# Kernel optimization log

Hardware: AMD Instinct MI355X
Metric: run time of the kernel (lower is better)

Reference implementation:

```python
import jax, jax.numpy as jnp
import numpy as np

N_NODES, N_EDGES, B = 5000, 160000, 8
IN_DIM, NB, RH = 64, 8, 64
MUL0, MUL1, MUL2 = 32, 16, 8
NW = 144  # 32*3 + 16*2 + 8*2 tensor-product path weights per edge
R_MAX, AVG_NEI = 6.0, 32.0
NL, POOL_H, OUT_D = 4, 128, 512


def setup_inputs():
    ks = jax.random.split(jax.random.key(0), 24)
    f = lambda k, shape, scale=1.0: jax.random.normal(k, shape, jnp.float32) * scale
    return {
        "x": f(ks[0], (N_NODES, IN_DIM)),
        "pos": f(ks[1], (N_NODES, 3)),
        "W_in": f(ks[2], (IN_DIM, MUL0), IN_DIM ** -0.5),
        "Wr1": f(ks[3], (NL, NB, RH), NB ** -0.5), "br1": jnp.zeros((NL, RH)),
        "Wr2": f(ks[4], (NL, RH, RH), RH ** -0.5), "br2": jnp.zeros((NL, RH)),
        "Wr3": f(ks[5], (NL, RH, NW), RH ** -0.5), "br3": jnp.zeros((NL, NW)),
        "Wm0": f(ks[6], (NL, 56, MUL0), 56 ** -0.5),
        "Wm1": f(ks[7], (NL, 48, MUL1), 48 ** -0.5),
        "Wm2": f(ks[8], (NL, 40, MUL2), 40 ** -0.5),
        "Ws0": f(ks[9], (NL, MUL0, MUL0), MUL0 ** -0.5),
        "Ws1": f(ks[10], (NL, MUL1, MUL1), MUL1 ** -0.5),
        "Ws2": f(ks[11], (NL, MUL2, MUL2), MUL2 ** -0.5),
        "Wg": f(ks[12], (NL, MUL0, MUL1 + MUL2), MUL0 ** -0.5), "bg": jnp.zeros((NL, MUL1 + MUL2)),
        "Wp1": f(ks[13], (MUL0, POOL_H), MUL0 ** -0.5), "bp1": jnp.zeros((POOL_H,)),
        "Wp2": f(ks[14], (POOL_H, POOL_H), POOL_H ** -0.5), "bp2": jnp.zeros((POOL_H,)),
        "Wp3": f(ks[15], (POOL_H, 1), POOL_H ** -0.5), "bp3": jnp.zeros((1,)),
        "Wo1": f(ks[16], (MUL0, OUT_D * 2), MUL0 ** -0.5), "bo1": jnp.zeros((OUT_D * 2,)),
        "g1": jnp.ones((OUT_D * 2,)), "be1": jnp.zeros((OUT_D * 2,)),
        "Wo2": f(ks[17], (OUT_D * 2, OUT_D), (OUT_D * 2) ** -0.5), "bo2": jnp.zeros((OUT_D,)),
        "g2": jnp.ones((OUT_D,)), "be2": jnp.zeros((OUT_D,)),
        "edge_index": jax.random.randint(ks[18], (2, N_EDGES), 0, N_NODES),
        "batch": jnp.sort(jax.random.randint(ks[19], (N_NODES,), 0, B)),
    }


def _ln(x, gamma, beta):
    m = x.mean(-1, keepdims=True)
    v = x.var(-1, keepdims=True)
    return (x - m) / jnp.sqrt(v + 1e-5) * gamma + beta


def _forward(x, pos, W_in, Wr1, br1, Wr2, br2, Wr3, br3, Wm0, Wm1, Wm2,
             Ws0, Ws1, Ws2, Wg, bg, Wp1, bp1, Wp2, bp2, Wp3, bp3,
             Wo1, bo1, g1, be1, Wo2, bo2, g2, be2, edge_index, batch):
    N = x.shape[0]
    src, dst = edge_index[0], edge_index[1]
    vec = pos[src] - pos[dst]                       # [E,3]
    r = jnp.sqrt(jnp.sum(vec * vec, -1) + 1e-12)    # [E]
    u = vec / r[:, None]
    # Bessel radial basis with smooth polynomial cutoff (p=6)
    nfreq = jnp.arange(1, NB + 1, dtype=x.dtype)
    bess = jnp.sqrt(2.0 / R_MAX) * jnp.sin(nfreq * jnp.pi * r[:, None] / R_MAX) / r[:, None]
    t = jnp.clip(r / R_MAX, 0.0, 1.0)
    fcut = (1.0 - 28.0 * t**6 + 48.0 * t**7 - 21.0 * t**8) * (r < R_MAX).astype(x.dtype)
    edge_emb = bess * fcut[:, None]                 # [E,NB]
    # real spherical harmonics of edge direction, component normalization
    ux, uy, uz = u[:, 0], u[:, 1], u[:, 2]
    Y1 = jnp.sqrt(3.0) * u                          # [E,3]
    Y2 = jnp.stack([15.0**0.5 * ux * uy, 15.0**0.5 * uy * uz,
                    0.5 * 5.0**0.5 * (3.0 * uz * uz - 1.0),
                    15.0**0.5 * ux * uz, 0.5 * 15.0**0.5 * (ux * ux - uy * uy)], -1)  # [E,5]
    # input embedding: 64x0e -> hidden irreps (only scalar path exists; l>0 start at 0)
    s = x @ W_in                                    # [N,32]
    v = jnp.zeros((N, MUL1, 3), x.dtype)            # [N,16,3] 1o
    q = jnp.zeros((N, MUL2, 5), x.dtype)            # [N,8,5]  2e
    for i in range(NL):
        w = jax.nn.silu(edge_emb @ Wr1[i] + br1[i])
        w = jax.nn.silu(w @ Wr2[i] + br2[i])
        w = w @ Wr3[i] + br3[i]                     # [E,144] per-edge TP path weights
        w_ss, w_sv, w_sq, w_vs, w_vv, w_qs, w_qq = jnp.split(w, [32, 64, 96, 112, 128, 136], -1)
        se, ve, qe = s[src], v[src], q[src]         # gather
        # tensor-product messages, grouped by output irrep
        m0 = jnp.concatenate([w_ss * se,
                              w_vv * jnp.einsum('ecm,em->ec', ve, Y1) / 3.0**0.5,
                              w_qq * jnp.einsum('ecm,em->ec', qe, Y2) / 5.0**0.5], -1)   # [E,56]
        m1 = jnp.concatenate([(w_sv * se)[:, :, None] * Y1[:, None, :],
                              w_vs[:, :, None] * ve], 1)                                  # [E,48,3]
        m2 = jnp.concatenate([(w_sq * se)[:, :, None] * Y2[:, None, :],
                              w_qs[:, :, None] * qe], 1)                                  # [E,40,5]
        a0 = jax.ops.segment_sum(m0, dst, num_segments=N) / AVG_NEI
        a1 = jax.ops.segment_sum(m1, dst, num_segments=N) / AVG_NEI
        a2 = jax.ops.segment_sum(m2, dst, num_segments=N) / AVG_NEI
        # per-irrep linear mix + self-connection
        ns = a0 @ Wm0[i] + s @ Ws0[i]
        nv = jnp.einsum('ncm,co->nom', a1, Wm1[i]) + jnp.einsum('ncm,co->nom', v, Ws1[i])
        nq = jnp.einsum('ncm,co->nom', a2, Wm2[i]) + jnp.einsum('ncm,co->nom', q, Ws2[i])
        # gate activation + resnet
        gates = jax.nn.sigmoid(ns @ Wg[i] + bg[i])  # [N,24]
        s = s + jax.nn.silu(ns)
        v = v + nv * gates[:, :MUL1, None]
        q = q + nq * gates[:, MUL1:, None]
    # attention pooling over scalar channels (scatter-softmax per graph)
    logits = (jax.nn.silu(jax.nn.silu(s @ Wp1 + bp1) @ Wp2 + bp2) @ Wp3 + bp3)[:, 0]
    mx = jax.ops.segment_max(logits, batch, num_segments=B)
    z = jnp.exp(logits - mx[batch])
    att = z / jax.ops.segment_sum(z, batch, num_segments=B)[batch]
    gpool = jax.ops.segment_sum(s * att[:, None], batch, num_segments=B)  # [B,32]
    h = jax.nn.silu(_ln(gpool @ Wo1 + bo1, g1, be1))
    return _ln(h @ Wo2 + bo2, g2, be2)              # [B,512]


def reference(x, pos, W_in, Wr1, br1, Wr2, br2, Wr3, br3, Wm0, Wm1, Wm2,
              Ws0, Ws1, Ws2, Wg, bg, Wp1, bp1, Wp2, bp2, Wp3, bp3,
              Wo1, bo1, g1, be1, Wo2, bo2, g2, be2, edge_index, batch):
    return _forward(x, pos, W_in, Wr1, br1, Wr2, br2, Wr3, br3, Wm0, Wm1, Wm2,
                    Ws0, Ws1, Ws2, Wg, bg, Wp1, bp1, Wp2, bp2, Wp3, bp3,
                    Wo1, bo1, g1, be1, Wo2, bo2, g2, be2, edge_index, batch)
```

## Files before the change

kernel.cpp:

```cpp
#include <hip/hip_runtime.h>

constexpr int NN  = 5000;
constexpr int NE  = 160000;
constexpr int NB_ = 8;
constexpr float RMAX   = 6.0f;
constexpr float INV_AVG = 1.0f/32.0f;
constexpr float SQ3  = 1.7320508075688772f;
constexpr float ISQ3 = 0.5773502691896258f;
constexpr float ISQ5 = 0.4472135954999579f;
constexpr float SQ15 = 3.872983346207417f;
constexpr float SQ5  = 2.2360679774997896f;
constexpr float PIF  = 3.14159265358979323846f;

__device__ __forceinline__ float sigmoid_f(float x){
    return 1.0f / (1.0f + __expf(-x));
}
__device__ __forceinline__ float silu_f(float x){ return x * sigmoid_f(x); }

__global__ void k_geom(const float* __restrict__ pos, const int* __restrict__ ei,
                       float* __restrict__ geom, int* __restrict__ counts){
    int e = blockIdx.x*256 + threadIdx.x;
    if (e >= NE) return;
    int s = ei[e], d = ei[NE + e];
    float vx = pos[3*s]-pos[3*d], vy = pos[3*s+1]-pos[3*d+1], vz = pos[3*s+2]-pos[3*d+2];
    float r2 = vx*vx + vy*vy + vz*vz + 1e-12f;
    float r  = sqrtf(r2);
    float ir = 1.0f/r;
    float ux = vx*ir, uy = vy*ir, uz = vz*ir;
    float t  = fminf(r*(1.0f/RMAX), 1.0f);
    float t2=t*t, t3=t2*t, t6=t3*t3, t7=t6*t, t8=t7*t;
    float fc = (1.0f - 28.0f*t6 + 48.0f*t7 - 21.0f*t8) * (r < RMAX ? 1.0f : 0.0f);
    float cb = sqrtf(2.0f/RMAX) * ir * fc;
    float w[16];
    #pragma unroll
    for (int k=0;k<8;k++){
        float arg = (float)(k+1) * (PIF/RMAX) * r;
        w[k] = cb * sinf(arg);
    }
    w[8]  = SQ3*ux; w[9] = SQ3*uy; w[10] = SQ3*uz;
    w[11] = SQ15*ux*uy; w[12] = SQ15*uy*uz; w[13] = 0.5f*SQ5*(3.0f*uz*uz-1.0f);
    w[14] = SQ15*ux*uz; w[15] = 0.5f*SQ15*(ux*ux-uy*uy);
    float4* o = (float4*)(geom + (size_t)e*16);
    o[0] = make_float4(w[0],w[1],w[2],w[3]);
    o[1] = make_float4(w[4],w[5],w[6],w[7]);
    o[2] = make_float4(w[8],w[9],w[10],w[11]);
    o[3] = make_float4(w[12],w[13],w[14],w[15]);
    atomicAdd(&counts[d], 1);
}

__global__ void k_scan(int* __restrict__ cr, int* __restrict__ fpos){
    __shared__ int part[256];
    int t = threadIdx.x;
    const int CH = (NN + 255)/256;
    int base = t*CH;
    int s = 0;
    for (int i=0;i<CH;i++){ int idx = base+i; if (idx < NN) s += cr[idx]; }
    part[t] = s; __syncthreads();
    for (int off=1; off<256; off<<=1){
        int v = (t >= off) ? part[t-off] : 0;
        __syncthreads();
        part[t] += v;
        __syncthreads();
    }
    int run = (t==0) ? 0 : part[t-1];
    for (int i=0;i<CH;i++){
        int idx = base+i;
        if (idx < NN){
            int c = cr[idx];
            cr[idx]  = run;
            fpos[idx] = run;
            run += c;
        } else if (idx == NN){
            cr[idx] = run;
        }
    }
}

__global__ void k_fill(const int* __restrict__ ei, int* __restrict__ fpos,
                       int* __restrict__ elist, int* __restrict__ slot){
    int e = blockIdx.x*256 + threadIdx.x;
    if (e >= NE) return;
    int d = ei[NE+e];
    int p = atomicAdd(&fpos[d], 1);
    elist[p] = e;
    slot[e]  = p;
}

__global__ void k_sinit(const float* __restrict__ x, const float* __restrict__ Win,
                        float* __restrict__ sA){
    int tid = blockIdx.x*256 + threadIdx.x;
    int n = tid >> 5, o = tid & 31;
    if (n >= NN) return;
    float a = 0.f;
    #pragma unroll
    for (int k=0;k<64;k++) a = fmaf(x[n*64+k], Win[k*32+o], a);
    sA[n*32+o] = a;
}

__launch_bounds__(256, 4)
__global__ void k_mlp(const float* __restrict__ geom, const int* __restrict__ slot,
                      const float* __restrict__ Wr1, const float* __restrict__ br1,
                      const float* __restrict__ Wr2, const float* __restrict__ br2,
                      const float* __restrict__ Wr3, const float* __restrict__ br3,
                      float* __restrict__ wbuf, int layer){
    __shared__ __align__(16) float w1s[8*64];
    __shared__ __align__(16) float w2s[64*64];
    __shared__ __align__(16) float b1s[64], b2s[64];
    __shared__ __align__(16) float b3s[144];
    __shared__ __align__(16) float embs[64][8];
    __shared__ __align__(16) float hs[64][68];
    __shared__ int   slots[64];

    const int t  = threadIdx.x;
    const int e0 = blockIdx.x * 64;
    const float* W1 = Wr1 + layer*(8*64);
    const float* b1 = br1 + layer*64;
    const float* W2 = Wr2 + layer*(64*64);
    const float* b2 = br2 + layer*64;
    const float* W3 = Wr3 + layer*(64*144);
    const float* b3 = br3 + layer*144;

    {
        const float4* W2v = (const float4*)W2;
        float4* w2v = (float4*)w2s;
        #pragma unroll
        for (int i=0;i<4;i++) w2v[t + 256*i] = W2v[t + 256*i];
        if (t < 128) ((float4*)w1s)[t] = ((const float4*)W1)[t];
        if (t < 64){ b1s[t] = b1[t]; b2s[t] = b2[t]; slots[t] = slot[e0 + t]; }
        if (t < 144) b3s[t] = b3[t];
        if (t < 128){
            ((float4*)embs)[t] = *((const float4*)geom + (size_t)(e0 + (t>>1))*4 + (t&1));
        }
    }
    __syncthreads();

    const int eg = t >> 3;
    const int jg = t & 7;
    const int ea = eg*2, eb = ea+1;

    float a0[2][8];
    #pragma unroll
    for (int i=0;i<2;i++)
        #pragma unroll
        for (int u=0;u<8;u++) a0[i][u] = b1s[8*jg+u];
    #pragma unroll
    for (int k=0;k<8;k++){
        float e_a = embs[ea][k], e_b = embs[eb][k];
        #pragma unroll
        for (int u=0;u<8;u++){
            float wv = w1s[k*64 + 8*jg + u];
            a0[0][u] = fmaf(e_a, wv, a0[0][u]);
            a0[1][u] = fmaf(e_b, wv, a0[1][u]);
        }
    }
    #pragma unroll
    for (int i=0;i<2;i++){
        int e = ea + i;
        float4 p0 = make_float4(silu_f(a0[i][0]), silu_f(a0[i][1]), silu_f(a0[i][2]), silu_f(a0[i][3]));
        float4 p1 = make_float4(silu_f(a0[i][4]), silu_f(a0[i][5]), silu_f(a0[i][6]), silu_f(a0[i][7]));
        *(float4*)&hs[e][8*jg]     = p0;
        *(float4*)&hs[e][8*jg + 4] = p1;
    }
    __syncthreads();

    float a1[2][8];
    #pragma unroll
    for (int i=0;i<2;i++)
        #pragma unroll
        for (int u=0;u<8;u++) a1[i][u] = b2s[8*jg+u];
    #pragma unroll
    for (int k=0;k<64;k++){
        float h_a = hs[ea][k], h_b = hs[eb][k];
        float4 wA = *(const float4*)&w2s[k*64 + 8*jg];
        float4 wB = *(const float4*)&w2s[k*64 + 8*jg + 4];
        a1[0][0]=fmaf(h_a,wA.x,a1[0][0]); a1[0][1]=fmaf(h_a,wA.y,a1[0][1]);
        a1[0][2]=fmaf(h_a,wA.z,a1[0][2]); a1[0][3]=fmaf(h_a,wA.w,a1[0][3]);
        a1[0][4]=fmaf(h_a,wB.x,a1[0][4]); a1[0][5]=fmaf(h_a,wB.y,a1[0][5]);
        a1[0][6]=fmaf(h_a,wB.z,a1[0][6]); a1[0][7]=fmaf(h_a,wB.w,a1[0][7]);
        a1[1][0]=fmaf(h_b,wA.x,a1[1][0]); a1[1][1]=fmaf(h_b,wA.y,a1[1][1]);
        a1[1][2]=fmaf(h_b,wA.z,a1[1][2]); a1[1][3]=fmaf(h_b,wA.w,a1[1][3]);
        a1[1][4]=fmaf(h_b,wB.x,a1[1][4]); a1[1][5]=fmaf(h_b,wB.y,a1[1][5]);
        a1[1][6]=fmaf(h_b,wB.z,a1[1][6]); a1[1][7]=fmaf(h_b,wB.w,a1[1][7]);
    }
    __syncthreads();
    #pragma unroll
    for (int i=0;i<2;i++){
        int e = ea + i;
        float4 p0 = make_float4(silu_f(a1[i][0]), silu_f(a1[i][1]), silu_f(a1[i][2]), silu_f(a1[i][3]));
        float4 p1 = make_float4(silu_f(a1[i][4]), silu_f(a1[i][5]), silu_f(a1[i][6]), silu_f(a1[i][7]));
        *(float4*)&hs[e][8*jg]     = p0;
        *(float4*)&hs[e][8*jg + 4] = p1;
    }
    __syncthreads();

    float c2[2][18];
    #pragma unroll
    for (int i=0;i<2;i++)
        #pragma unroll
        for (int u=0;u<18;u++) c2[i][u] = b3s[18*jg+u];

    float* w3c = w2s;
    for (int ch=0; ch<4; ++ch){
        const float4* src = (const float4*)(W3 + 16*ch*144);
        float4* dst = (float4*)w3c;
        dst[t]       = src[t];
        dst[t+256]   = src[t+256];
        if (t < 64) dst[t+512] = src[t+512];
        __syncthreads();
        #pragma unroll
        for (int kk=0;kk<16;kk++){
            int k = 16*ch + kk;
            float h_a = hs[ea][k], h_b = hs[eb][k];
            #pragma unroll
            for (int u2=0;u2<9;u2++){
                float2 wv = *(const float2*)&w3c[kk*144 + 18*jg + 2*u2];
                c2[0][2*u2]   = fmaf(h_a, wv.x, c2[0][2*u2]);
                c2[0][2*u2+1] = fmaf(h_a, wv.y, c2[0][2*u2+1]);
                c2[1][2*u2]   = fmaf(h_b, wv.x, c2[1][2*u2]);
                c2[1][2*u2+1] = fmaf(h_b, wv.y, c2[1][2*u2+1]);
            }
        }
        __syncthreads();
    }
    #pragma unroll
    for (int i=0;i<2;i++){
        float* wo = wbuf + (size_t)slots[ea+i]*144 + 18*jg;
        #pragma unroll
        for (int u2=0;u2<9;u2++)
            *(float2*)(wo + 2*u2) = make_float2(c2[i][2*u2], c2[i][2*u2+1]);
    }
}

__launch_bounds__(512, 4)
__global__ void k_gather(const int* __restrict__ rowp, const int* __restrict__ elist,
                         const int* __restrict__ ei, const float* __restrict__ geom,
                         const float* __restrict__ wbuf,
                         const float* __restrict__ s_in, const float* __restrict__ v_in,
                         const float* __restrict__ q_in,
                         float* __restrict__ s_out, float* __restrict__ v_out,
                         float* __restrict__ q_out,
                         const float* __restrict__ Wm0, const float* __restrict__ Wm1,
                         const float* __restrict__ Wm2,
                         const float* __restrict__ Ws0, const float* __restrict__ Ws1,
                         const float* __restrict__ Ws2,
                         const float* __restrict__ Wg, const float* __restrict__ bg,
                         int layer){
    __shared__ float pacc[8][400];
    __shared__ float lacc[400];
    __shared__ float lns[32];
    __shared__ float lgate[24];
    const int n = blockIdx.x;
    const int t = threadIdx.x;
    const int w = t >> 6;
    const int lane = t & 63;

    int s0_w, s0_o, s0_ob;
    if (lane < 32){ s0_w = lane;            s0_o = lane;          s0_ob = lane; }
    else if (lane < 48){ s0_w = 112+(lane-32); s0_o = 3*(lane-32); s0_ob = lane; }
    else if (lane < 56){ s0_w = 136+(lane-48); s0_o = 5*(lane-48); s0_ob = lane; }
    else { int R = lane-56; s0_w = 32+R; s0_o = R; s0_ob = 56+3*R; }
    int s1_w, s1_o, s1_ob;
    if (lane < 24){ int R = lane+8; s1_w = 32+R; s1_o = R;     s1_ob = 56+3*R; }
    else if (lane < 40){ int j = lane-24; s1_w = 96+j; s1_o = 3*j; s1_ob = 152+3*j; }
    else { int R = lane-40; s1_w = 64+R; s1_o = R; s1_ob = 200+5*R; }
    int s2_w, s2_o, s2_ob;
    if (lane < 8){ int R = lane+24; s2_w = 64+R; s2_o = R;   s2_ob = 200+5*R; }
    else { int j = lane-8; s2_w = 128+j; s2_o = 5*j; s2_ob = 360+5*j; }

    float a0[3] = {0.f,0.f,0.f};
    float a1[5] = {0.f,0.f,0.f,0.f,0.f};
    float a2[5] = {0.f,0.f,0.f,0.f,0.f};

    auto body = [&](int idx){
        int e   = elist[idx];
        int src = ei[e];
        const float* gp = geom + (size_t)e*16;
        float4 y14 = *(const float4*)(gp + 8);
        float4 y58 = *(const float4*)(gp + 12);
        const float* wp = wbuf + (size_t)idx*144;
        const float* sp = s_in + (size_t)src*32;
        const float* vp = v_in + (size_t)src*48;
        const float* qp = q_in + (size_t)src*40;
        {
            float wv = wp[s0_w];
            if (lane < 32){
                a0[0] = fmaf(wv, sp[s0_o], a0[0]);
            } else if (lane < 48){
                float dv = vp[s0_o]*y14.x + vp[s0_o+1]*y14.y + vp[s0_o+2]*y14.z;
                a0[0] = fmaf(wv*ISQ3, dv, a0[0]);
            } else if (lane < 56){
                float dq = qp[s0_o]*y14.w + qp[s0_o+1]*y58.x + qp[s0_o+2]*y58.y
                         + qp[s0_o+3]*y58.z + qp[s0_o+4]*y58.w;
                a0[0] = fmaf(wv*ISQ5, dq, a0[0]);
            } else {
                float tmp = wv * sp[s0_o];
                a0[0] = fmaf(tmp, y14.x, a0[0]);
                a0[1] = fmaf(tmp, y14.y, a0[1]);
                a0[2] = fmaf(tmp, y14.z, a0[2]);
            }
        }
        {
            float wv = wp[s1_w];
            if (lane < 24){
                float tmp = wv * sp[s1_o];
                a1[0] = fmaf(tmp, y14.x, a1[0]);
                a1[1] = fmaf(tmp, y14.y, a1[1]);
                a1[2] = fmaf(tmp, y14.z, a1[2]);
            } else if (lane < 40){
                a1[0] = fmaf(wv, vp[s1_o],   a1[0]);
                a1[1] = fmaf(wv, vp[s1_o+1], a1[1]);
                a1[2] = fmaf(wv, vp[s1_o+2], a1[2]);
            } else {
                float tmp = wv * sp[s1_o];
                a1[0] = fmaf(tmp, y14.w, a1[0]);
                a1[1] = fmaf(tmp, y58.x, a1[1]);
                a1[2] = fmaf(tmp, y58.y, a1[2]);
                a1[3] = fmaf(tmp, y58.z, a1[3]);
                a1[4] = fmaf(tmp, y58.w, a1[4]);
            }
        }
        if (lane < 16){
            float wv = wp[s2_w];
            if (lane < 8){
                float tmp = wv * sp[s2_o];
                a2[0] = fmaf(tmp, y14.w, a2[0]);
                a2[1] = fmaf(tmp, y58.x, a2[1]);
                a2[2] = fmaf(tmp, y58.y, a2[2]);
                a2[3] = fmaf(tmp, y58.z, a2[3]);
                a2[4] = fmaf(tmp, y58.w, a2[4]);
            } else {
                a2[0] = fmaf(wv, qp[s2_o],   a2[0]);
                a2[1] = fmaf(wv, qp[s2_o+1], a2[1]);
                a2[2] = fmaf(wv, qp[s2_o+2], a2[2]);
                a2[3] = fmaf(wv, qp[s2_o+3], a2[3]);
                a2[4] = fmaf(wv, qp[s2_o+4], a2[4]);
            }
        }
    };

    const int beg = rowp[n], end = rowp[n+1];
    int idx = beg + w;
    for (; idx + 8 < end; idx += 16){
        body(idx);
        body(idx + 8);
    }
    if (idx < end) body(idx);

    pacc[w][s0_ob] = a0[0];
    if (lane >= 56){ pacc[w][s0_ob+1] = a0[1]; pacc[w][s0_ob+2] = a0[2]; }
    pacc[w][s1_ob] = a1[0]; pacc[w][s1_ob+1] = a1[1]; pacc[w][s1_ob+2] = a1[2];
    if (lane >= 40){ pacc[w][s1_ob+3] = a1[3]; pacc[w][s1_ob+4] = a1[4]; }
    if (lane < 16){
        #pragma unroll
        for (int u=0;u<5;u++) pacc[w][s2_ob+u] = a2[u];
    }
    __syncthreads();
    for (int c=t; c<400; c+=512){
        float s8 = 0.f;
        #pragma unroll
        for (int g=0; g<8; g++) s8 += pacc[g][c];
        lacc[c] = s8 * INV_AVG;
    }
    __syncthreads();

    const float* Wm0p = Wm0 + layer*(56*32);
    const float* Ws0p = Ws0 + layer*(32*32);
    const float* Wm1p = Wm1 + layer*(48*16);
    const float* Ws1p = Ws1 + layer*(16*16);
    const float* Wm2p = Wm2 + layer*(40*8);
    const float* Ws2p = Ws2 + layer*(8*8);
    const float* Wgp  = Wg  + layer*(32*24);
    const float* bgp  = bg  + layer*24;

    float nvv = 0.f, nqv = 0.f;
    if (t < 32){
        float a = 0.f;
        #pragma unroll
        for (int c=0;c<56;c++) a = fmaf(lacc[c], Wm0p[c*32+t], a);
        #pragma unroll
        for (int c=0;c<32;c++) a = fmaf(s_in[n*32+c], Ws0p[c*32+t], a);
        lns[t] = a;
    } else if (t >= 64 && t < 112){
        int o = t-64, o3 = o/3, m3 = o-3*o3;
        #pragma unroll
        for (int c=0;c<48;c++) nvv = fmaf(lacc[56+c*3+m3], Wm1p[c*16+o3], nvv);
        #pragma unroll
        for (int c=0;c<16;c++) nvv = fmaf(v_in[n*48+c*3+m3], Ws1p[c*16+o3], nvv);
    } else if (t >= 128 && t < 168){
        int o = t-128, o5 = o/5, m5 = o-5*o5;
        #pragma unroll
        for (int c=0;c<40;c++) nqv = fmaf(lacc[200+c*5+m5], Wm2p[c*8+o5], nqv);
        #pragma unroll
        for (int c=0;c<8;c++)  nqv = fmaf(q_in[n*40+c*5+m5], Ws2p[c*8+o5], nqv);
    }
    __syncthreads();
    if (t < 24){
        float a = bgp[t];
        #pragma unroll
        for (int c=0;c<32;c++) a = fmaf(lns[c], Wgp[c*24+t], a);
        lgate[t] = sigmoid_f(a);
    }
    __syncthreads();
    if (t < 32){
        s_out[n*32+t] = s_in[n*32+t] + silu_f(lns[t]);
    } else if (t >= 64 && t < 112){
        int o = t-64;
        v_out[n*48+o] = v_in[n*48+o] + nvv * lgate[o/3];
    } else if (t >= 128 && t < 168){
        int o = t-128;
        q_out[n*40+o] = q_in[n*40+o] + nqv * lgate[16+o/5];
    }
}

__launch_bounds__(128)
__global__ void k_pool(const float* __restrict__ s_in,
                       const float* __restrict__ Wp1, const float* __restrict__ bp1,
                       const float* __restrict__ Wp2, const float* __restrict__ bp2,
                       const float* __restrict__ Wp3, const float* __restrict__ bp3,
                       float* __restrict__ logits){
    __shared__ float ls[32];
    __shared__ float lh[128];
    __shared__ float wred[2];
    int n = blockIdx.x, t = threadIdx.x;
    if (t < 32) ls[t] = s_in[n*32+t];
    __syncthreads();
    float a = bp1[t];
    #pragma unroll
    for (int c=0;c<32;c++) a = fmaf(ls[c], Wp1[c*128+t], a);
    lh[t] = silu_f(a);
    __syncthreads();
    float b = bp2[t];
    #pragma unroll
    for (int k=0;k<128;k++) b = fmaf(lh[k], Wp2[k*128+t], b);
    float p = silu_f(b) * Wp3[t];
    #pragma unroll
    for (int off=32; off>0; off>>=1) p += __shfl_down(p, off, 64);
    if ((t & 63) == 0) wred[t>>6] = p;
    __syncthreads();
    if (t == 0) logits[n] = wred[0] + wred[1] + bp3[0];
}

__global__ void k_ranges(const int* __restrict__ batch, int* __restrict__ rs, int* __restrict__ re){
    int n = blockIdx.x*256 + threadIdx.x;
    if (n >= NN) return;
    int b = batch[n];
    if (n == 0 || batch[n-1] != b) rs[b] = n;
    if (n == NN-1 || batch[n+1] != b) re[b] = n+1;
}

__launch_bounds__(1024)
__global__ void k_spool(const float* __restrict__ logits, const float* __restrict__ s_in,
                        const int* __restrict__ rs, const int* __restrict__ re,
                        float* __restrict__ gpool){
    __shared__ float red[1024];
    __shared__ float racc[32*33];
    __shared__ float dred[32];
    __shared__ float smx;
    int b = blockIdx.x, t = threadIdx.x;
    int lo = rs[b], hi = re[b];
    float m = -3.0e38f;
    for (int n = lo + t; n < hi; n += 1024) m = fmaxf(m, logits[n]);
    red[t] = m; __syncthreads();
    for (int s2=512; s2>0; s2>>=1){ if (t<s2) red[t] = fmaxf(red[t], red[t+s2]); __syncthreads(); }
    if (t==0) smx = red[0];
    __syncthreads();
    float mx = smx;
    int g = t >> 5, c = t & 31;
    float acc = 0.f, zs = 0.f;
    for (int n = lo + g; n < hi; n += 32){
        float z = __expf(logits[n] - mx);
        acc = fmaf(z, s_in[n*32+c], acc);
        zs += z;
    }
    racc[g*33+c] = acc;
    if (c == 0) dred[g] = zs;
    __syncthreads();
    if (t < 32){
        float a = 0.f, d = 0.f;
        #pragma unroll
        for (int g2=0; g2<32; g2++){ a += racc[g2*33+t]; d += dred[g2]; }
        gpool[b*32+t] = a / d;
    }
}

__launch_bounds__(1024)
__global__ void k_out1(const float* __restrict__ gpool, const float* __restrict__ Wo1,
                       const float* __restrict__ bo1, const float* __restrict__ g1,
                       const float* __restrict__ be1, float* __restrict__ hbuf){
    __shared__ float lg[32];
    __shared__ float red[1024];
    __shared__ float stats[2];
    int b = blockIdx.x, t = threadIdx.x;
    if (t < 32) lg[t] = gpool[b*32+t];
    __syncthreads();
    float a = bo1[t];
    #pragma unroll
    for (int c=0;c<32;c++) a = fmaf(lg[c], Wo1[c*1024+t], a);
    red[t] = a; __syncthreads();
    for (int s2=512; s2>0; s2>>=1){ if (t<s2) red[t]+=red[t+s2]; __syncthreads(); }
    if (t==0) stats[0] = red[0]*(1.0f/1024.0f);
    __syncthreads();
    float mean = stats[0];
    float d = a - mean;
    red[t] = d*d; __syncthreads();
    for (int s2=512; s2>0; s2>>=1){ if (t<s2) red[t]+=red[t+s2]; __syncthreads(); }
    if (t==0) stats[1] = red[0]*(1.0f/1024.0f);
    __syncthreads();
    float rstd = rsqrtf(stats[1] + 1e-5f);
    hbuf[b*1024+t] = silu_f(d*rstd*g1[t] + be1[t]);
}

__launch_bounds__(1024)
__global__ void k_out2(const float* __restrict__ hbuf, const float* __restrict__ Wo2,
                       const float* __restrict__ bo2, const float* __restrict__ g2,
                       const float* __restrict__ be2, float* __restrict__ out){
    __shared__ float lh[1024];
    __shared__ float part[1024];
    __shared__ float red[1024];
    __shared__ float stats[2];
    int b = blockIdx.x, t = threadIdx.x;
    lh[t] = hbuf[b*1024 + t];
    __syncthreads();
    int j = t & 511, half = t >> 9;
    float a = (half == 0) ? bo2[j] : 0.0f;
    int k0 = half*512;
    #pragma unroll 8
    for (int k=0;k<512;k++) a = fmaf(lh[k0+k], Wo2[(size_t)(k0+k)*512 + j], a);
    part[t] = a; __syncthreads();
    float y = 0.f;
    if (t < 512) y = part[t] + part[t+512];
    red[t] = (t < 512) ? y : 0.f; __syncthreads();
    for (int s2=512; s2>0; s2>>=1){ if (t<s2) red[t]+=red[t+s2]; __syncthreads(); }
    if (t==0) stats[0] = red[0]*(1.0f/512.0f);
    __syncthreads();
    float mean = stats[0];
    float d = y - mean;
    red[t] = (t < 512) ? d*d : 0.f; __syncthreads();
    for (int s2=512; s2>0; s2>>=1){ if (t<s2) red[t]+=red[t+s2]; __syncthreads(); }
    if (t==0) stats[1] = red[0]*(1.0f/512.0f);
    __syncthreads();
    float rstd = rsqrtf(stats[1] + 1e-5f);
    if (t < 512) out[b*512+t] = d*rstd*g2[t] + be2[t];
}

extern "C" void kernel_launch(void* const* d_in, const int* in_sizes, int n_in,
                              void* d_out, int out_size, void* d_ws, size_t ws_size,
                              hipStream_t stream){
    const float* x   = (const float*)d_in[0];
    const float* pos = (const float*)d_in[1];
    const float* Win = (const float*)d_in[2];
    const float* Wr1 = (const float*)d_in[3];
    const float* br1 = (const float*)d_in[4];
    const float* Wr2 = (const float*)d_in[5];
    const float* br2 = (const float*)d_in[6];
    const float* Wr3 = (const float*)d_in[7];
    const float* br3 = (const float*)d_in[8];
    const float* Wm0 = (const float*)d_in[9];
    const float* Wm1 = (const float*)d_in[10];
    const float* Wm2 = (const float*)d_in[11];
    const float* Ws0 = (const float*)d_in[12];
    const float* Ws1 = (const float*)d_in[13];
    const float* Ws2 = (const float*)d_in[14];
    const float* Wg  = (const float*)d_in[15];
    const float* bg  = (const float*)d_in[16];
    const float* Wp1 = (const float*)d_in[17];
    const float* bp1 = (const float*)d_in[18];
    const float* Wp2 = (const float*)d_in[19];
    const float* bp2 = (const float*)d_in[20];
    const float* Wp3 = (const float*)d_in[21];
    const float* bp3 = (const float*)d_in[22];
    const float* Wo1 = (const float*)d_in[23];
    const float* bo1 = (const float*)d_in[24];
    const float* g1  = (const float*)d_in[25];
    const float* be1 = (const float*)d_in[26];
    const float* Wo2 = (const float*)d_in[27];
    const float* bo2 = (const float*)d_in[28];
    const float* g2  = (const float*)d_in[29];
    const float* be2 = (const float*)d_in[30];
    const int* ei    = (const int*)d_in[31];
    const int* batch = (const int*)d_in[32];
    float* out = (float*)d_out;

    char* wsb = (char*)d_ws;
    size_t off = 0;
    auto take = [&](size_t bytes)->char*{
        char* p = wsb + off;
        off = (off + bytes + 255) & ~(size_t)255;
        return p;
    };
    float* geom  = (float*)take((size_t)NE*16*4);
    float* wbuf  = (float*)take((size_t)NE*144*4);
    int*   rowp  = (int*)take((size_t)(NN+1)*4);
    int*   fpos  = (int*)take((size_t)NN*4);
    int*   elist = (int*)take((size_t)NE*4);
    int*   slot  = (int*)take((size_t)NE*4);
    float* vA = (float*)take((size_t)NN*48*4);
    float* qA = (float*)take((size_t)NN*40*4);
    float* sA = (float*)take((size_t)NN*32*4);
    float* sB = (float*)take((size_t)NN*32*4);
    float* vB = (float*)take((size_t)NN*48*4);
    float* qB = (float*)take((size_t)NN*40*4);
    float* logits = (float*)take((size_t)NN*4);
    int*   rs     = (int*)take(64);
    int*   re     = rs + 8;
    float* gpool  = (float*)take((size_t)NB_*32*4);
    float* hbuf   = (float*)take((size_t)NB_*1024*4);
    (void)ws_size; (void)in_sizes; (void)n_in; (void)out_size;

    hipMemsetAsync(rowp, 0, (size_t)(NN+1)*4, stream);
    hipMemsetAsync(vA,   0, (size_t)NN*48*4 + (size_t)NN*40*4, stream);
    hipMemsetAsync(rs,   0, 64, stream);

    k_geom<<<(NE+255)/256, 256, 0, stream>>>(pos, ei, geom, rowp);
    k_scan<<<1, 256, 0, stream>>>(rowp, fpos);
    k_fill<<<(NE+255)/256, 256, 0, stream>>>(ei, fpos, elist, slot);
    k_sinit<<<(NN*32+255)/256, 256, 0, stream>>>(x, Win, sA);
    k_ranges<<<(NN+255)/256, 256, 0, stream>>>(batch, rs, re);

    float* si=sA; float* so=sB; float* vi=vA; float* vo=vB; float* qi=qA; float* qo=qB;
    for (int layer=0; layer<4; ++layer){
        k_mlp<<<NE/64, 256, 0, stream>>>(geom, slot, Wr1, br1, Wr2, br2, Wr3, br3, wbuf, layer);
        k_gather<<<NN, 512, 0, stream>>>(rowp, elist, ei, geom, wbuf, si, vi, qi, so, vo, qo,
                                         Wm0, Wm1, Wm2, Ws0, Ws1, Ws2, Wg, bg, layer);
        float* ts=si; si=so; so=ts;
        float* tv=vi; vi=vo; vo=tv;
        float* tq=qi; qi=qo; qo=tq;
    }
    k_pool<<<NN, 128, 0, stream>>>(si, Wp1, bp1, Wp2, bp2, Wp3, bp3, logits);
    k_spool<<<NB_, 1024, 0, stream>>>(logits, si, rs, re, gpool);
    k_out1<<<NB_, 1024, 0, stream>>>(gpool, Wo1, bo1, g1, be1, hbuf);
    k_out2<<<NB_, 1024, 0, stream>>>(hbuf, Wo2, bo2, g2, be2, out);
}
```

Baseline: 1.097 ms.

## Pack edge harmonics and source index into dst-sorted weight rows; halve gather block

The MLP kernel now also writes each edge's eight spherical-harmonic values into a padded 160-float row of the weight buffer, stored in destination-sorted order. k_fill writes the source node index in sorted order, so the gather no longer goes through elist, ei and geom for each edge. This removes two dependent random loads plus a scattered geom read per edge, in exchange for a slightly larger weight buffer write. The gather block also drops from 8 to 4 wavefronts, with 8 blocks per CU allowed, which trades intra-node parallelism for occupancy.

```diff
diff --git a/kernel.cpp b/kernel.cpp
--- a/kernel.cpp
+++ b/kernel.cpp
@@ -3,6 +3,7 @@
 constexpr int NN  = 5000;
 constexpr int NE  = 160000;
 constexpr int NB_ = 8;
+constexpr int WROW = 160;
 constexpr float RMAX   = 6.0f;
 constexpr float INV_AVG = 1.0f/32.0f;
 constexpr float SQ3  = 1.7320508075688772f;
@@ -77,13 +78,13 @@
 }
 
 __global__ void k_fill(const int* __restrict__ ei, int* __restrict__ fpos,
-                       int* __restrict__ elist, int* __restrict__ slot){
+                       int* __restrict__ slot, int* __restrict__ srcp){
     int e = blockIdx.x*256 + threadIdx.x;
     if (e >= NE) return;
     int d = ei[NE+e];
     int p = atomicAdd(&fpos[d], 1);
-    elist[p] = e;
     slot[e]  = p;
+    srcp[p]  = ei[e];
 }
 
 __global__ void k_sinit(const float* __restrict__ x, const float* __restrict__ Win,
@@ -224,16 +225,20 @@
     }
     #pragma unroll
     for (int i=0;i<2;i++){
-        float* wo = wbuf + (size_t)slots[ea+i]*144 + 18*jg;
+        float* wo = wbuf + (size_t)slots[ea+i]*WROW + 18*jg;
         #pragma unroll
         for (int u2=0;u2<9;u2++)
             *(float2*)(wo + 2*u2) = make_float2(c2[i][2*u2], c2[i][2*u2+1]);
     }
-}
-
-__launch_bounds__(512, 4)
-__global__ void k_gather(const int* __restrict__ rowp, const int* __restrict__ elist,
-                         const int* __restrict__ ei, const float* __restrict__ geom,
+    if (t < 128){
+        int e = t >> 1, half = t & 1;
+        *(float4*)(wbuf + (size_t)slots[e]*WROW + 144 + half*4) =
+            *((const float4*)geom + (size_t)(e0+e)*4 + 2 + half);
+    }
+}
+
+__launch_bounds__(256, 8)
+__global__ void k_gather(const int* __restrict__ rowp, const int* __restrict__ srcp,
                          const float* __restrict__ wbuf,
                          const float* __restrict__ s_in, const float* __restrict__ v_in,
                          const float* __restrict__ q_in,
@@ -245,7 +250,7 @@
                          const float* __restrict__ Ws2,
                          const float* __restrict__ Wg, const float* __restrict__ bg,
                          int layer){
-    __shared__ float pacc[8][400];
+    __shared__ float pacc[4][400];
     __shared__ float lacc[400];
     __shared__ float lns[32];
     __shared__ float lgate[24];
@@ -272,12 +277,10 @@
     float a2[5] = {0.f,0.f,0.f,0.f,0.f};
 
     auto body = [&](int idx){
-        int e   = elist[idx];
-        int src = ei[e];
-        const float* gp = geom + (size_t)e*16;
-        float4 y14 = *(const float4*)(gp + 8);
-        float4 y58 = *(const float4*)(gp + 12);
-        const float* wp = wbuf + (size_t)idx*144;
+        const float* wp = wbuf + (size_t)idx*WROW;
+        int src = srcp[idx];
+        float4 y14 = *(const float4*)(wp + 144);
+        float4 y58 = *(const float4*)(wp + 148);
         const float* sp = s_in + (size_t)src*32;
         const float* vp = v_in + (size_t)src*48;
         const float* qp = q_in + (size_t)src*40;
@@ -340,9 +343,9 @@
 
     const int beg = rowp[n], end = rowp[n+1];
     int idx = beg + w;
-    for (; idx + 8 < end; idx += 16){
+    for (; idx + 4 < end; idx += 8){
         body(idx);
-        body(idx + 8);
+        body(idx + 4);
     }
     if (idx < end) body(idx);
 
@@ -355,12 +358,8 @@
         for (int u=0;u<5;u++) pacc[w][s2_ob+u] = a2[u];
     }
     __syncthreads();
-    for (int c=t; c<400; c+=512){
-        float s8 = 0.f;
-        #pragma unroll
-        for (int g=0; g<8; g++) s8 += pacc[g][c];
-        lacc[c] = s8 * INV_AVG;
-    }
+    for (int c=t; c<400; c+=256)
+        lacc[c] = (pacc[0][c]+pacc[1][c]+pacc[2][c]+pacc[3][c]) * INV_AVG;
     __syncthreads();
 
     const float* Wm0p = Wm0 + layer*(56*32);
@@ -589,11 +588,11 @@
         return p;
     };
     float* geom  = (float*)take((size_t)NE*16*4);
-    float* wbuf  = (float*)take((size_t)NE*144*4);
+    float* wbuf  = (float*)take((size_t)NE*WROW*4);
     int*   rowp  = (int*)take((size_t)(NN+1)*4);
     int*   fpos  = (int*)take((size_t)NN*4);
-    int*   elist = (int*)take((size_t)NE*4);
     int*   slot  = (int*)take((size_t)NE*4);
+    int*   srcp  = (int*)take((size_t)NE*4);
     float* vA = (float*)take((size_t)NN*48*4);
     float* qA = (float*)take((size_t)NN*40*4);
     float* sA = (float*)take((size_t)NN*32*4);
@@ -613,14 +612,14 @@
 
     k_geom<<<(NE+255)/256, 256, 0, stream>>>(pos, ei, geom, rowp);
     k_scan<<<1, 256, 0, stream>>>(rowp, fpos);
-    k_fill<<<(NE+255)/256, 256, 0, stream>>>(ei, fpos, elist, slot);
+    k_fill<<<(NE+255)/256, 256, 0, stream>>>(ei, fpos, slot, srcp);
     k_sinit<<<(NN*32+255)/256, 256, 0, stream>>>(x, Win, sA);
     k_ranges<<<(NN+255)/256, 256, 0, stream>>>(batch, rs, re);
 
     float* si=sA; float* so=sB; float* vi=vA; float* vo=vB; float* qi=qA; float* qo=qB;
     for (int layer=0; layer<4; ++layer){
         k_mlp<<<NE/64, 256, 0, stream>>>(geom, slot, Wr1, br1, Wr2, br2, Wr3, br3, wbuf, layer);
-        k_gather<<<NN, 512, 0, stream>>>(rowp, elist, ei, geom, wbuf, si, vi, qi, so, vo, qo,
+        k_gather<<<NN, 256, 0, stream>>>(rowp, srcp, wbuf, si, vi, qi, so, vo, qo,
                                          Wm0, Wm1, Wm2, Ws0, Ws1, Ws2, Wg, bg, layer);
         float* ts=si; si=so; so=ts;
         float* tv=vi; vi=vo; vo=tv;
```

Result: faster. 1.006 ms (-8.3%).
